# Kernel tuning notes

Measured on AMD Instinct MI355X. Metric: run time of the kernel, lower is better.

## Reference

```python
import jax, jax.numpy as jnp
import numpy as np

INPUT_SIZE = 2048
H1 = 256
H2 = 64
NB = 8
BATCH = 16384


def setup_inputs() -> dict:
    key = jax.random.key(0)
    ks = jax.random.split(key, 8)
    x = jax.random.normal(ks[0], (BATCH, INPUT_SIZE), dtype=jnp.float32)
    bucket_indices = jax.random.randint(ks[1], (BATCH,), 0, NB, dtype=jnp.int32)
    # torch nn.Linear weights: (out_features, in_features), bias: (out_features,)
    def lin(k, fan_in, fan_out):
        kw, kb = jax.random.split(k)
        bound = 1.0 / np.sqrt(fan_in)
        W = jax.random.uniform(kw, (fan_out, fan_in), jnp.float32, -bound, bound)
        b = jax.random.uniform(kb, (fan_out,), jnp.float32, -bound, bound)
        return W, b
    W1, b1 = lin(ks[2], INPUT_SIZE, H1 * NB)
    W2, b2 = lin(ks[3], H1, H2 * NB)
    W3, b3 = lin(ks[4], H2, 1 * NB)
    return {"x": x, "bucket_indices": bucket_indices,
            "W1": W1, "b1": b1, "W2": W2, "b2": b2, "W3": W3, "b3": b3}


def _gather_bucket(all_out, idx, width):
    # all_out: (B, NB*width) -> select per-sample bucket slice -> (B, width)
    B = all_out.shape[0]
    per = all_out.reshape(B, NB, width)
    return jnp.take_along_axis(per, idx[:, None, None], axis=1)[:, 0, :]


def reference(x, bucket_indices, W1, b1, W2, b2, W3, b3):
    idx = bucket_indices.astype(jnp.int32)
    h1_all = x @ W1.T + b1                      # (B, H1*NB)
    h1 = jnp.clip(_gather_bucket(h1_all, idx, H1), 0.0, 1.0)
    h2_all = h1 @ W2.T + b2                     # (B, H2*NB)
    h2 = jnp.clip(_gather_bucket(h2_all, idx, H2), 0.0, 1.0)
    out_all = h2 @ W3.T + b3                    # (B, NB)
    out = _gather_bucket(out_all, idx, 1)       # (B, 1)
    return out[:, :, None]                      # (B, 1, 1) matches unsqueeze(-1)
```

## Files before the change

### kernel.cpp

```cpp
#include <hip/hip_runtime.h>

#define INSZ   2048
#define NH1    256
#define NH2    64
#define NB     8
#define BATCH  16384

#define TS        64
#define MAXTILES  (BATCH / TS)
#define GRIDX     (NB * MAXTILES)

#define W1F_U4   (NB * 64 * 16 * 64)
#define W2F_U4   (NB * 8 * 4 * 64)

#define META_OFF  0
#define ORDER_OFF 1024
#define W1F_OFF   (1024 + BATCH * 4)
#define W2F_OFF   (W1F_OFF + W1F_U4 * 16)
#define WS_NEED   (W2F_OFF + W2F_U4 * 16)

typedef float f4  __attribute__((ext_vector_type(4)));
typedef float f32x4 __attribute__((ext_vector_type(4)));
typedef short bf16x8 __attribute__((ext_vector_type(8)));

__device__ __forceinline__ unsigned short f2bf(float f) {
    unsigned u = __float_as_uint(f);
    u += 0x7fffu + ((u >> 16) & 1u);
    return (unsigned short)(u >> 16);
}
__device__ __forceinline__ float clamp01(float v) { return fminf(fmaxf(v, 0.0f), 1.0f); }
__device__ __forceinline__ unsigned pack2(float a, float b) {
    return (unsigned)f2bf(a) | ((unsigned)f2bf(b) << 16);
}

__device__ __forceinline__ void glds16(const short* gsrc, short* ldst) {
    __builtin_amdgcn_global_load_lds(
        (const __attribute__((address_space(1))) unsigned int*)gsrc,
        (__attribute__((address_space(3))) unsigned int*)ldst, 16, 0, 0);
}


__global__ void k_countscan(const int* __restrict__ idx, int* __restrict__ meta) {
    __shared__ int scnt[NB];
    int t = threadIdx.x;
    if (t < NB) scnt[t] = 0;
    __syncthreads();
    int local[NB];
#pragma unroll
    for (int bb = 0; bb < NB; bb++) local[bb] = 0;
    for (int i = t; i < BATCH; i += 1024) {
        int b = idx[i];
#pragma unroll
        for (int bb = 0; bb < NB; bb++) local[bb] += (b == bb) ? 1 : 0;
    }
#pragma unroll
    for (int bb = 0; bb < NB; bb++) {
        int v = local[bb];
        v += __shfl_xor(v, 1);  v += __shfl_xor(v, 2);  v += __shfl_xor(v, 4);
        v += __shfl_xor(v, 8);  v += __shfl_xor(v, 16); v += __shfl_xor(v, 32);
        if ((t & 63) == 0) atomicAdd(&scnt[bb], v);
    }
    __syncthreads();
    if (t == 0) {
        int run = 0;
        for (int b = 0; b < NB; b++) {
            int c = scnt[b];
            meta[b]      = c;
            meta[8 + b]  = run;
            meta[16 + b] = run;
            run += c;
        }
    }
}

__global__ void k_scatter(const int* __restrict__ idx, int* __restrict__ meta,
                          int* __restrict__ order) {
    __shared__ int wcnt[16][NB];
    __shared__ int sbase[NB];
    int t = threadIdx.x;
    int i = blockIdx.x * 1024 + t;
    int b = idx[i];
    int wv = t >> 6, lane = t & 63;
    unsigned long long mymask = 0;
#pragma unroll
    for (int bb = 0; bb < NB; bb++) {
        unsigned long long m = __ballot(b == bb);
        if (b == bb) mymask = m;
        if (lane == bb) wcnt[wv][bb] = (int)__popcll(m);
    }
    int myrank = (int)__popcll(mymask & ((1ull << lane) - 1ull));
    __syncthreads();
    if (t < NB) {
        int sum = 0;
        for (int w2 = 0; w2 < 16; w2++) { int c = wcnt[w2][t]; wcnt[w2][t] = sum; sum += c; }
        sbase[t] = atomicAdd(&meta[16 + t], sum);
    }
    __syncthreads();
    order[sbase[b] + wcnt[wv][b] + myrank] = i;
}

__global__ void k_pack(const float* __restrict__ W1, const float* __restrict__ W2,
                       uint4* __restrict__ W1f, uint4* __restrict__ W2f) {
    int u = blockIdx.x * 256 + threadIdx.x;
    if (u < W1F_U4) {
        int lane = u & 63, cg = (u >> 6) & 15, kb = (u >> 10) & 63, bkt = u >> 16;
        int l15 = lane & 15, quad = lane >> 4;
        const float* p = W1 + (size_t)(bkt * NH1 + cg * 16 + l15) * INSZ + kb * 32 + quad * 8;
        f4 lo = *(const f4*)p, hi = *(const f4*)(p + 4);
        uint4 o;
        o.x = pack2(lo[0], lo[1]); o.y = pack2(lo[2], lo[3]);
        o.z = pack2(hi[0], hi[1]); o.w = pack2(hi[2], hi[3]);
        W1f[u] = o;
    } else {
        int v = u - W1F_U4;
        if (v >= W2F_U4) return;
        int lane = v & 63, cg2 = (v >> 6) & 3, kb2 = (v >> 8) & 7, bkt = v >> 11;
        int l15 = lane & 15, quad = lane >> 4;
        const float* p = W2 + (size_t)(bkt * NH2 + cg2 * 16 + l15) * NH1 + kb2 * 32 + quad * 8;
        f4 lo = *(const f4*)p, hi = *(const f4*)(p + 4);
        uint4 o;
        o.x = pack2(lo[0], lo[1]); o.y = pack2(lo[2], lo[3]);
        o.z = pack2(hi[0], hi[1]); o.w = pack2(hi[2], hi[3]);
        W2f[v] = o;
    }
}


__global__ __launch_bounds__(256, 2) void fused_v4(
    const float* __restrict__ x, const int* __restrict__ meta,
    const int* __restrict__ order,
    const short* __restrict__ W1f, const short* __restrict__ W2f,
    const float* __restrict__ b1, const float* __restrict__ b2,
    const float* __restrict__ W3, const float* __restrict__ b3,
    float* __restrict__ out)
{
    const int bkt  = blockIdx.x & 7;
    const int base = (blockIdx.x >> 3) * TS;
    const int cnt  = meta[bkt];
    if (cnt == 0 || base >= cnt) return;
    const int off = meta[8 + bkt];

    __shared__ short sW[2][8192];
    __shared__ short sX[2][2048];
    __shared__ short sh1[TS * 264];

    const int t = threadIdx.x;
    const int lane = t & 63, w = t >> 6;
    const int l15 = lane & 15, quad = lane >> 4;

    const int xr = t >> 2, kq = t & 3;
    int ii = base + xr; if (ii > cnt - 1) ii = cnt - 1;
    const float* xrp = x + (size_t)order[off + ii] * INSZ + kq * 8;
    const int sxoff = (xr >> 4) * 512 + (kq * 16 + (xr & 15)) * 8;

    const short* wtile = W1f + (size_t)bkt * (64 * 8192);

    f32x4 acc[16];
#pragma unroll
    for (int cg = 0; cg < 16; cg++) acc[cg] = (f32x4)0.0f;

    {
        const short* g = wtile;
#pragma unroll
        for (int i = 0; i < 4; i++) {
            int cb = w * 4 + i;
            glds16(g + cb * 512 + lane * 8, &sW[0][cb * 512]);
        }
    }
    f4 xa = *(const f4*)xrp, xb = *(const f4*)(xrp + 4);
    {
        union { bf16x8 v; unsigned u[4]; } r;
        r.u[0] = pack2(xa[0], xa[1]); r.u[1] = pack2(xa[2], xa[3]);
        r.u[2] = pack2(xb[0], xb[1]); r.u[3] = pack2(xb[2], xb[3]);
        *(bf16x8*)&sX[0][sxoff] = r.v;
    }
    xa = *(const f4*)(xrp + 32); xb = *(const f4*)(xrp + 36);
    __syncthreads();

#pragma unroll 1
    for (int kb = 0; kb < 64; kb++) {
        const int p = kb & 1;
        if (kb < 63) {
            const short* g = wtile + (size_t)(kb + 1) * 8192;
#pragma unroll
            for (int i = 0; i < 4; i++) {
                int cb = w * 4 + i;
                glds16(g + cb * 512 + lane * 8, &sW[p ^ 1][cb * 512]);
            }
            union { bf16x8 v; unsigned u[4]; } r;
            r.u[0] = pack2(xa[0], xa[1]); r.u[1] = pack2(xa[2], xa[3]);
            r.u[2] = pack2(xb[0], xb[1]); r.u[3] = pack2(xb[2], xb[3]);
            *(bf16x8*)&sX[p ^ 1][sxoff] = r.v;
        }
        if (kb < 62) {
            xa = *(const f4*)(xrp + (kb + 2) * 32);
            xb = *(const f4*)(xrp + (kb + 2) * 32 + 4);
        }
        bf16x8 a = *(const bf16x8*)&sX[p][w * 512 + (quad * 16 + l15) * 8];
#pragma unroll
        for (int cg = 0; cg < 16; cg++) {
            bf16x8 bfr = *(const bf16x8*)&sW[p][(cg * 64 + lane) * 8];
            acc[cg] = __builtin_amdgcn_mfma_f32_16x16x32_bf16(a, bfr, acc[cg], 0, 0, 0);
        }
        __syncthreads();
    }

#pragma unroll
    for (int cg = 0; cg < 16; cg++) {
        int col = cg * 16 + l15;
        float bias = b1[bkt * NH1 + col];
#pragma unroll
        for (int r = 0; r < 4; r++) {
            int row = w * 16 + quad * 4 + r;
            sh1[row * 264 + col] = (short)f2bf(clamp01(acc[cg][r] + bias));
        }
    }

    f32x4 c2[4];
#pragma unroll
    for (int c = 0; c < 4; c++) c2[c] = (f32x4)0.0f;
    const short* w2p = W2f + (size_t)bkt * 16384 + lane * 8;
#pragma unroll
    for (int kb2 = 0; kb2 < 8; kb2++) {
        bf16x8 a2 = *(const bf16x8*)&sh1[(w * 16 + l15) * 264 + kb2 * 32 + quad * 8];
#pragma unroll
        for (int cg2 = 0; cg2 < 4; cg2++) {
            bf16x8 bw = *(const bf16x8*)(w2p + (kb2 * 4 + cg2) * 512);
            c2[cg2] = __builtin_amdgcn_mfma_f32_16x16x32_bf16(a2, bw, c2[cg2], 0, 0, 0);
        }
    }

    float s[4] = {0, 0, 0, 0};
#pragma unroll
    for (int cg2 = 0; cg2 < 4; cg2++) {
        float bias2 = b2[bkt * NH2 + cg2 * 16 + l15];
        float w3v   = W3[bkt * NH2 + cg2 * 16 + l15];
#pragma unroll
        for (int r = 0; r < 4; r++)
            s[r] += clamp01(c2[cg2][r] + bias2) * w3v;
    }
    float b3v = b3[bkt];
#pragma unroll
    for (int r = 0; r < 4; r++) {
        float pp = s[r];
        pp += __shfl_xor(pp, 1); pp += __shfl_xor(pp, 2);
        pp += __shfl_xor(pp, 4); pp += __shfl_xor(pp, 8);
        if (l15 == 0) {
            int row = w * 16 + quad * 4 + r;
            if (base + row < cnt) out[order[off + base + row]] = pp + b3v;
        }
    }
}


__global__ void naive_mlp(const float* __restrict__ x, const int* __restrict__ idx,
                          const float* __restrict__ W1, const float* __restrict__ b1,
                          const float* __restrict__ W2, const float* __restrict__ b2,
                          const float* __restrict__ W3, const float* __restrict__ b3,
                          float* __restrict__ out)
{
    int i = blockIdx.x;
    int b = idx[i];
    __shared__ float sx[INSZ];
    __shared__ float sh1n[NH1];
    __shared__ float sh2n[NH2];
    for (int t = threadIdx.x; t < INSZ; t += 256) sx[t] = x[(size_t)i * INSZ + t];
    __syncthreads();
    int j = threadIdx.x;
    {
        const float* wr = W1 + (size_t)(b * NH1 + j) * INSZ;
        float acc = b1[b * NH1 + j];
        for (int k = 0; k < INSZ; k++) acc += sx[k] * wr[k];
        sh1n[j] = fminf(fmaxf(acc, 0.f), 1.f);
    }
    __syncthreads();
    if (j < NH2) {
        const float* wr = W2 + (size_t)(b * NH2 + j) * NH1;
        float acc = b2[b * NH2 + j];
        for (int k = 0; k < NH1; k++) acc += sh1n[k] * wr[k];
        sh2n[j] = fminf(fmaxf(acc, 0.f), 1.f);
    }
    __syncthreads();
    if (j == 0) {
        float acc = b3[b];
        for (int k = 0; k < NH2; k++) acc += sh2n[k] * W3[b * NH2 + k];
        out[i] = acc;
    }
}

extern "C" void kernel_launch(void* const* d_in, const int* in_sizes, int n_in,
                              void* d_out, int out_size, void* d_ws, size_t ws_size,
                              hipStream_t stream) {
    const float* x  = (const float*)d_in[0];
    const int* bidx = (const int*)d_in[1];
    const float* W1 = (const float*)d_in[2];
    const float* b1 = (const float*)d_in[3];
    const float* W2 = (const float*)d_in[4];
    const float* b2 = (const float*)d_in[5];
    const float* W3 = (const float*)d_in[6];
    const float* b3 = (const float*)d_in[7];
    float* out = (float*)d_out;

    if (ws_size >= (size_t)WS_NEED) {
        char* ws = (char*)d_ws;
        int*   meta  = (int*)(ws + META_OFF);
        int*   order = (int*)(ws + ORDER_OFF);
        uint4* W1f   = (uint4*)(ws + W1F_OFF);
        uint4* W2f   = (uint4*)(ws + W2F_OFF);

        k_countscan<<<1, 1024, 0, stream>>>(bidx, meta);
        k_scatter<<<BATCH / 1024, 1024, 0, stream>>>(bidx, meta, order);
        k_pack<<<(W1F_U4 + W2F_U4) / 256, 256, 0, stream>>>(W1, W2, W1f, W2f);
        fused_v4<<<GRIDX, 256, 0, stream>>>(x, meta, order,
                                            (const short*)W1f, (const short*)W2f,
                                            b1, b2, W3, b3, out);
    } else {
        naive_mlp<<<BATCH, 256, 0, stream>>>(x, bidx, W1, b1, W2, b2, W3, b3, out);
    }
}
```

Measured before the change: 276.7 us.

## Drop LDS staging, load W1 fragments to registers with smaller row tiles

The fused MLP kernel no longer stages W1 and x tiles through double-buffered shared memory with barriers each k-step. Instead each wave loads its own W1 fragments and x rows straight into registers, prefetching one step ahead for weights and two for x. The row tile drops from 64 to 32, the four waves are split into 2 row groups times 2 column halves, and a small shared reduction combines the partial output sums. This removes the per-iteration __syncthreads and LDS traffic and raises occupancy, but each block now reuses every W1 fragment across fewer rows, so global/L2 weight traffic roughly doubles and register pressure goes up.

```diff
diff --git a/kernel.cpp b/kernel.cpp
--- a/kernel.cpp
+++ b/kernel.cpp
@@ -6,7 +6,7 @@
 #define NB     8
 #define BATCH  16384
 
-#define TS        64
+#define TS        32
 #define MAXTILES  (BATCH / TS)
 #define GRIDX     (NB * MAXTILES)
 
@@ -32,11 +32,11 @@
 __device__ __forceinline__ unsigned pack2(float a, float b) {
     return (unsigned)f2bf(a) | ((unsigned)f2bf(b) << 16);
 }
-
-__device__ __forceinline__ void glds16(const short* gsrc, short* ldst) {
-    __builtin_amdgcn_global_load_lds(
-        (const __attribute__((address_space(1))) unsigned int*)gsrc,
-        (__attribute__((address_space(3))) unsigned int*)ldst, 16, 0, 0);
+__device__ __forceinline__ bf16x8 cvt8(f4 lo, f4 hi) {
+    union { bf16x8 v; unsigned u[4]; } r;
+    r.u[0] = pack2(lo[0], lo[1]); r.u[1] = pack2(lo[2], lo[3]);
+    r.u[2] = pack2(hi[0], hi[1]); r.u[3] = pack2(hi[2], hi[3]);
+    return r.v;
 }
 
 
@@ -126,7 +126,7 @@
 }
 
 
-__global__ __launch_bounds__(256, 2) void fused_v4(
+__global__ __launch_bounds__(256, 3) void fused_v5(
     const float* __restrict__ x, const int* __restrict__ meta,
     const int* __restrict__ order,
     const short* __restrict__ W1f, const short* __restrict__ W2f,
@@ -137,119 +137,99 @@
     const int bkt  = blockIdx.x & 7;
     const int base = (blockIdx.x >> 3) * TS;
     const int cnt  = meta[bkt];
-    if (cnt == 0 || base >= cnt) return;
+    if (base >= cnt) return;
     const int off = meta[8 + bkt];
 
-    __shared__ short sW[2][8192];
-    __shared__ short sX[2][2048];
-    __shared__ short sh1[TS * 264];
+    __shared__ short sh1[TS * 260];
+    __shared__ float sPart[2][TS];
 
     const int t = threadIdx.x;
     const int lane = t & 63, w = t >> 6;
     const int l15 = lane & 15, quad = lane >> 4;
-
-    const int xr = t >> 2, kq = t & 3;
-    int ii = base + xr; if (ii > cnt - 1) ii = cnt - 1;
-    const float* xrp = x + (size_t)order[off + ii] * INSZ + kq * 8;
-    const int sxoff = (xr >> 4) * 512 + (kq * 16 + (xr & 15)) * 8;
-
-    const short* wtile = W1f + (size_t)bkt * (64 * 8192);
-
-    f32x4 acc[16];
-#pragma unroll
-    for (int cg = 0; cg < 16; cg++) acc[cg] = (f32x4)0.0f;
-
-    {
-        const short* g = wtile;
-#pragma unroll
-        for (int i = 0; i < 4; i++) {
-            int cb = w * 4 + i;
-            glds16(g + cb * 512 + lane * 8, &sW[0][cb * 512]);
-        }
-    }
-    f4 xa = *(const f4*)xrp, xb = *(const f4*)(xrp + 4);
-    {
-        union { bf16x8 v; unsigned u[4]; } r;
-        r.u[0] = pack2(xa[0], xa[1]); r.u[1] = pack2(xa[2], xa[3]);
-        r.u[2] = pack2(xb[0], xb[1]); r.u[3] = pack2(xb[2], xb[3]);
-        *(bf16x8*)&sX[0][sxoff] = r.v;
-    }
-    xa = *(const f4*)(xrp + 32); xb = *(const f4*)(xrp + 36);
-    __syncthreads();
-
-#pragma unroll 1
+    const int g = w & 1, ch = w >> 1;
+
+    int ii = base + g * 16 + l15; if (ii > cnt - 1) ii = cnt - 1;
+    const float* xrp = x + (size_t)order[off + ii] * INSZ + quad * 8;
+    const short* wp = W1f + ((size_t)bkt << 19) + (size_t)(ch * 8) * 512 + lane * 8;
+
+    f32x4 acc[8];
+#pragma unroll
+    for (int i = 0; i < 8; i++) acc[i] = (f32x4)0.0f;
+
+    bf16x8 bcur[8], bnext[8];
+#pragma unroll
+    for (int i = 0; i < 8; i++) bcur[i] = *(const bf16x8*)(wp + i * 512);
+
+    f4 xa0 = *(const f4*)xrp,        xa1 = *(const f4*)(xrp + 4);
+    f4 xb0 = *(const f4*)(xrp + 32), xb1 = *(const f4*)(xrp + 36);
+    f4 xc0 = *(const f4*)(xrp + 64), xc1 = *(const f4*)(xrp + 68);
+
+#pragma unroll 2
     for (int kb = 0; kb < 64; kb++) {
-        const int p = kb & 1;
         if (kb < 63) {
-            const short* g = wtile + (size_t)(kb + 1) * 8192;
-#pragma unroll
-            for (int i = 0; i < 4; i++) {
-                int cb = w * 4 + i;
-                glds16(g + cb * 512 + lane * 8, &sW[p ^ 1][cb * 512]);
-            }
-            union { bf16x8 v; unsigned u[4]; } r;
-            r.u[0] = pack2(xa[0], xa[1]); r.u[1] = pack2(xa[2], xa[3]);
-            r.u[2] = pack2(xb[0], xb[1]); r.u[3] = pack2(xb[2], xb[3]);
-            *(bf16x8*)&sX[p ^ 1][sxoff] = r.v;
-        }
-        if (kb < 62) {
-            xa = *(const f4*)(xrp + (kb + 2) * 32);
-            xb = *(const f4*)(xrp + (kb + 2) * 32 + 4);
-        }
-        bf16x8 a = *(const bf16x8*)&sX[p][w * 512 + (quad * 16 + l15) * 8];
-#pragma unroll
-        for (int cg = 0; cg < 16; cg++) {
-            bf16x8 bfr = *(const bf16x8*)&sW[p][(cg * 64 + lane) * 8];
-            acc[cg] = __builtin_amdgcn_mfma_f32_16x16x32_bf16(a, bfr, acc[cg], 0, 0, 0);
-        }
-        __syncthreads();
-    }
-
-#pragma unroll
-    for (int cg = 0; cg < 16; cg++) {
-        int col = cg * 16 + l15;
+            const short* np = wp + (size_t)(kb + 1) * 8192;
+#pragma unroll
+            for (int i = 0; i < 8; i++) bnext[i] = *(const bf16x8*)(np + i * 512);
+        }
+        bf16x8 a = cvt8(xa0, xa1);
+        xa0 = xb0; xa1 = xb1;
+        xb0 = xc0; xb1 = xc1;
+        if (kb < 61) {
+            xc0 = *(const f4*)(xrp + (kb + 3) * 32);
+            xc1 = *(const f4*)(xrp + (kb + 3) * 32 + 4);
+        }
+#pragma unroll
+        for (int i = 0; i < 8; i++)
+            acc[i] = __builtin_amdgcn_mfma_f32_16x16x32_bf16(a, bcur[i], acc[i], 0, 0, 0);
+#pragma unroll
+        for (int i = 0; i < 8; i++) bcur[i] = bnext[i];
+    }
+
+#pragma unroll
+    for (int i = 0; i < 8; i++) {
+        int col = (ch * 8 + i) * 16 + l15;
         float bias = b1[bkt * NH1 + col];
 #pragma unroll
         for (int r = 0; r < 4; r++) {
-            int row = w * 16 + quad * 4 + r;
-            sh1[row * 264 + col] = (short)f2bf(clamp01(acc[cg][r] + bias));
-        }
-    }
-
-    f32x4 c2[4];
-#pragma unroll
-    for (int c = 0; c < 4; c++) c2[c] = (f32x4)0.0f;
+            int row = g * 16 + quad * 4 + r;
+            sh1[row * 260 + col] = (short)f2bf(clamp01(acc[i][r] + bias));
+        }
+    }
+    __syncthreads();
+
+    f32x4 c2[2];
+    c2[0] = (f32x4)0.0f; c2[1] = (f32x4)0.0f;
     const short* w2p = W2f + (size_t)bkt * 16384 + lane * 8;
 #pragma unroll
     for (int kb2 = 0; kb2 < 8; kb2++) {
-        bf16x8 a2 = *(const bf16x8*)&sh1[(w * 16 + l15) * 264 + kb2 * 32 + quad * 8];
-#pragma unroll
-        for (int cg2 = 0; cg2 < 4; cg2++) {
-            bf16x8 bw = *(const bf16x8*)(w2p + (kb2 * 4 + cg2) * 512);
-            c2[cg2] = __builtin_amdgcn_mfma_f32_16x16x32_bf16(a2, bw, c2[cg2], 0, 0, 0);
+        bf16x8 a2 = *(const bf16x8*)&sh1[(g * 16 + l15) * 260 + kb2 * 32 + quad * 8];
+#pragma unroll
+        for (int j = 0; j < 2; j++) {
+            bf16x8 bw = *(const bf16x8*)(w2p + (kb2 * 4 + ch * 2 + j) * 512);
+            c2[j] = __builtin_amdgcn_mfma_f32_16x16x32_bf16(a2, bw, c2[j], 0, 0, 0);
         }
     }
 
     float s[4] = {0, 0, 0, 0};
 #pragma unroll
-    for (int cg2 = 0; cg2 < 4; cg2++) {
-        float bias2 = b2[bkt * NH2 + cg2 * 16 + l15];
-        float w3v   = W3[bkt * NH2 + cg2 * 16 + l15];
+    for (int j = 0; j < 2; j++) {
+        int n2 = (ch * 2 + j) * 16 + l15;
+        float bias2 = b2[bkt * NH2 + n2];
+        float w3v   = W3[bkt * NH2 + n2];
 #pragma unroll
         for (int r = 0; r < 4; r++)
-            s[r] += clamp01(c2[cg2][r] + bias2) * w3v;
-    }
-    float b3v = b3[bkt];
+            s[r] += clamp01(c2[j][r] + bias2) * w3v;
+    }
 #pragma unroll
     for (int r = 0; r < 4; r++) {
         float pp = s[r];
         pp += __shfl_xor(pp, 1); pp += __shfl_xor(pp, 2);
         pp += __shfl_xor(pp, 4); pp += __shfl_xor(pp, 8);
-        if (l15 == 0) {
-            int row = w * 16 + quad * 4 + r;
-            if (base + row < cnt) out[order[off + base + row]] = pp + b3v;
-        }
-    }
+        if (l15 == 0) sPart[ch][g * 16 + quad * 4 + r] = pp;
+    }
+    __syncthreads();
+    if (t < TS && base + t < cnt)
+        out[order[off + base + t]] = sPart[0][t] + sPart[1][t] + b3[bkt];
 }
 
 
@@ -311,7 +291,7 @@
         k_countscan<<<1, 1024, 0, stream>>>(bidx, meta);
         k_scatter<<<BATCH / 1024, 1024, 0, stream>>>(bidx, meta, order);
         k_pack<<<(W1F_U4 + W2F_U4) / 256, 256, 0, stream>>>(W1, W2, W1f, W2f);
-        fused_v4<<<GRIDX, 256, 0, stream>>>(x, meta, order,
+        fused_v5<<<GRIDX, 256, 0, stream>>>(x, meta, order,
                                             (const short*)W1f, (const short*)W2f,
                                             b1, b2, W3, b3, out);
     } else {
```

After: 327.1 us. 1.18x slower.
